# Performance work log

Hardware: AMD Instinct MI355X
Metric: run time of the kernel (lower is better)

## Reference

```python
import jax, jax.numpy as jnp
import numpy as np
import jax.ops

N = 100000   # nodes
E = 3200000  # edges
B = 256      # graphs in batch
F_IN, H, C = 128, 64, 2


def gcn_conv(x, src, dst, W, b):
    # PyG GCNConv: x' = D^{-1/2} (A + I) D^{-1/2} (x W) + b
    n = x.shape[0]
    h = x @ W  # [N, H]
    loop = jnp.arange(n)
    s = jnp.concatenate([src, loop])  # add self-loops
    d = jnp.concatenate([dst, loop])
    deg = jax.ops.segment_sum(jnp.ones_like(d, dtype=h.dtype), d, num_segments=n)
    dinv = jnp.where(deg > 0, jax.lax.rsqrt(deg), 0.0)
    norm = dinv[s] * dinv[d]  # [E+N]
    msg = h[s] * norm[:, None]  # gather + scale
    out = jax.ops.segment_sum(msg, d, num_segments=n)  # scatter-add
    return out + b


def setup_inputs() -> dict:
    key = jax.random.key(0)
    ks = jax.random.split(key, 10)
    x = jax.random.normal(ks[0], (N, F_IN), dtype=jnp.float32)
    edge_index = jax.random.randint(ks[1], (2, E), 0, N, dtype=jnp.int64)
    batch = jnp.sort(jax.random.randint(ks[2], (N,), 0, B, dtype=jnp.int64))
    glorot = lambda k, fi, fo: jax.random.uniform(k, (fi, fo), jnp.float32, -1, 1) * np.sqrt(6.0 / (fi + fo))
    return {
        "x": x, "edge_index": edge_index, "batch": batch,
        "W1": glorot(ks[3], F_IN, H), "b1": jnp.zeros((H,), jnp.float32),
        "W2": glorot(ks[4], H, H), "b2": jnp.zeros((H,), jnp.float32),
        "Wl": glorot(ks[5], H, C), "bl": jnp.zeros((C,), jnp.float32),
    }


def reference(x, edge_index, batch, W1, b1, W2, b2, Wl, bl):
    src, dst = edge_index[0], edge_index[1]
    h = jax.nn.relu(gcn_conv(x, src, dst, W1, b1))
    h = jax.nn.relu(gcn_conv(h, src, dst, W2, b2))
    # global_mean_pool over graph ids
    sums = jax.ops.segment_sum(h, batch, num_segments=B)
    cnt = jax.ops.segment_sum(jnp.ones((h.shape[0],), h.dtype), batch, num_segments=B)
    pooled = sums / jnp.maximum(cnt, 1.0)[:, None]  # [B, H]
    return pooled @ Wl + bl  # [B, C]
```

## Files before the change

kernel.cpp:

```cpp
#include <hip/hip_runtime.h>
#include <hip/hip_bf16.h>


#define HDIM 64
#define NB 256
#define SGRID 256

typedef __attribute__((ext_vector_type(8))) short short8;
typedef __attribute__((ext_vector_type(4))) float f32x4;
typedef __attribute__((ext_vector_type(2))) float f32x2;
union FragU { uint4 u; short8 s; };

static __device__ __forceinline__ unsigned bf16_bits(float f) {
    unsigned u = __float_as_uint(f);
    return (u + 0x7fff + ((u >> 16) & 1)) >> 16;
}
static __device__ __forceinline__ float bflo(unsigned w) { return __uint_as_float(w << 16); }
static __device__ __forceinline__ float bfhi(unsigned w) { return __uint_as_float(w & 0xffff0000u); }


__global__ __launch_bounds__(1024) void k_bcount(const int* __restrict__ dst,
        int* __restrict__ blkhist, int E, int npb, int chunk) {
    __shared__ int lh[NB];
    int tid = threadIdx.x;
    if (tid < NB) lh[tid] = 0;
    __syncthreads();
    int e0 = blockIdx.x * chunk, e1 = min(E, e0 + chunk);
    for (int e = e0 + tid; e < e1; e += 1024)
        atomicAdd(&lh[(unsigned)dst[e] / (unsigned)npb], 1);
    __syncthreads();
    if (tid < NB) blkhist[blockIdx.x * NB + tid] = lh[tid];
}

__global__ void k_bscan2(int* __restrict__ blkhist, int* __restrict__ bcnt) {
    __shared__ int s[SGRID];
    int b = blockIdx.x, t = threadIdx.x;
    int orig = blkhist[t * NB + b];
    s[t] = orig;
    __syncthreads();
    for (int off = 1; off < SGRID; off <<= 1) {
        int v = 0;
        if (t >= off) v = s[t - off];
        __syncthreads();
        s[t] += v;
        __syncthreads();
    }
    blkhist[t * NB + b] = s[t] - orig;
    if (t == SGRID - 1) bcnt[b] = s[t];
}

__global__ __launch_bounds__(1024) void k_bscan_prep(const int* __restrict__ bcnt,
        int* __restrict__ bstart, const float* __restrict__ W1,
        const float* __restrict__ W2, uint4* __restrict__ W1s, uint4* __restrict__ W2s,
        unsigned* __restrict__ hsbA, unsigned* __restrict__ hsbB, int N) {
    __shared__ int s[NB];
    int t = threadIdx.x;
    int orig = 0;
    if (t < NB) { orig = bcnt[t]; s[t] = orig; }
    __syncthreads();
    for (int off = 1; off < NB; off <<= 1) {
        int v = 0;
        if (t < NB && t >= off) v = s[t - off];
        __syncthreads();
        if (t < NB) s[t] += v;
        __syncthreads();
    }
    if (t < NB) bstart[t] = s[t] - orig;
    if (t == NB - 1) bstart[NB] = s[t];
    int lane = t & 63, ci = t >> 6;
    {
        int kt = ci >> 2, nt = ci & 3;
        int kbase = kt * 32 + (lane >> 4) * 8;
        int n = nt * 16 + (lane & 15);
        uint4 o;
        unsigned* op = (unsigned*)&o;
        for (int jj = 0; jj < 4; ++jj) {
            unsigned lo = bf16_bits(W1[(kbase + 2 * jj) * 64 + n]);
            unsigned hi = bf16_bits(W1[(kbase + 2 * jj + 1) * 64 + n]);
            op[jj] = lo | (hi << 16);
        }
        W1s[ci * 64 + lane] = o;
    }
    if (ci < 8) {
        int kt = ci >> 2, nt = ci & 3;
        int kbase = kt * 32 + (lane >> 4) * 8;
        int n = nt * 16 + (lane & 15);
        uint4 o;
        unsigned* op = (unsigned*)&o;
        for (int jj = 0; jj < 4; ++jj) {
            unsigned lo = bf16_bits(W2[(kbase + 2 * jj) * 64 + n]);
            unsigned hi = bf16_bits(W2[(kbase + 2 * jj + 1) * 64 + n]);
            op[jj] = lo | (hi << 16);
        }
        W2s[ci * 64 + lane] = o;
    }
    if (t < 32) hsbA[(size_t)N * 32 + t] = 0;
    else if (t < 64) hsbB[(size_t)N * 32 + (t - 32)] = 0;
}

__global__ __launch_bounds__(1024) void k_bscatter(const int* __restrict__ src,
        const int* __restrict__ dst, const int* __restrict__ bstart,
        const int* __restrict__ blkhist, unsigned* __restrict__ ebuf,
        int E, int npb, int chunk) {
    __shared__ int base[NB], lcur[NB];
    int tid = threadIdx.x;
    if (tid < NB) {
        base[tid] = bstart[tid] + blkhist[blockIdx.x * NB + tid];
        lcur[tid] = 0;
    }
    __syncthreads();
    int e0 = blockIdx.x * chunk, e1 = min(E, e0 + chunk);
    for (int e = e0 + tid; e < e1; e += 1024) {
        int d = dst[e];
        unsigned b = (unsigned)d / (unsigned)npb;
        unsigned ld = (unsigned)d - b * (unsigned)npb;
        int off = atomicAdd(&lcur[b], 1);
        ebuf[base[b] + off] = (ld << 17) | (unsigned)src[e];
    }
}

__global__ __launch_bounds__(1024) void k_bfill(const unsigned* __restrict__ ebuf,
        const int* __restrict__ bstart, int4* __restrict__ meta,
        float* __restrict__ dinv, int* __restrict__ csr, int N, int npb) {
    __shared__ int h[512], p[512], c[512];
    int b = blockIdx.x, tid = threadIdx.x;
    int vlo = b * npb;
    int vcnt = min(npb, N - vlo);
    if (vcnt <= 0) return;
    for (int i = tid; i < 512; i += 1024) h[i] = 0;
    __syncthreads();
    int e0 = bstart[b], e1 = bstart[b + 1];
    for (int e = e0 + tid; e < e1; e += 1024)
        atomicAdd(&h[ebuf[e] >> 17], 1);
    __syncthreads();
    int pc = 0;
    if (tid < 512) {
        pc = (tid < vcnt) ? ((h[tid] + 7) & ~7) : 0;
        p[tid] = pc;
    }
    __syncthreads();
    for (int off = 1; off < 512; off <<= 1) {
        int v = 0;
        if (tid < 512 && tid >= off) v = p[tid - off];
        __syncthreads();
        if (tid < 512) p[tid] += v;
        __syncthreads();
    }
    int bb = e0 + 7 * vlo;
    if (tid < vcnt) {
        int excl = p[tid] - pc;
        int v = vlo + tid;
        float di = rsqrtf((float)(h[tid] + 1));
        meta[v] = make_int4(bb + excl, pc >> 3, __float_as_int(di), 0);
        dinv[v] = di;
        c[tid] = excl;
    }
    __syncthreads();
    for (int e = e0 + tid; e < e1; e += 1024) {
        unsigned ed = ebuf[e];
        int off = atomicAdd(&c[ed >> 17], 1);
        csr[bb + off] = (int)(ed & 0x1FFFFu);
    }
    __syncthreads();
    if (tid < vcnt) {
        int excl = p[tid] - pc;
        for (int q = excl + h[tid]; q < excl + pc; ++q) csr[bb + q] = N;
    }
}

#define MFMA_EPILOGUE(OUT)                                                     \
    {                                                                          \
        int col = lane & 15;                                                   \
        float dv[4];                                                           \
        for (int r = 0; r < 4; ++r) {                                          \
            int vr = v0 + quad * 4 + r;                                        \
            dv[r] = dinv[vr < n ? vr : (n - 1)];                               \
        }                                                                      \
        for (int nt = 0; nt < 4; ++nt)                                         \
            for (int r = 0; r < 4; ++r) {                                      \
                int vr = v0 + quad * 4 + r;                                    \
                float val = acc[nt][r] * dv[r];                                \
                float oth = __shfl_xor(val, 1, 64);                            \
                if (!(lane & 1) && vr < n)                                     \
                    OUT[(size_t)vr * 32 + nt * 8 + (col >> 1)] =               \
                        bf16_bits(val) | (bf16_bits(oth) << 16);               \
            }                                                                  \
    }

__global__ __launch_bounds__(256) void k_mgemm1(const float* __restrict__ X,
        const uint4* __restrict__ W1s, const float* __restrict__ dinv,
        unsigned* __restrict__ hsb, int n) {
    __shared__ float Xs[4][16 * 132];
    int lane = threadIdx.x & 63, wv = threadIdx.x >> 6;
    int v0 = (blockIdx.x * 4 + wv) * 16;
    if (v0 >= n) return;
    const float4* X4 = (const float4*)X;
#pragma unroll
    for (int i = 0; i < 8; ++i) {
        int gi = i * 64 + lane;
        int r = gi >> 5, c4 = gi & 31;
        int vr = v0 + r; if (vr >= n) vr = n - 1;
        float4 t = X4[(size_t)vr * 32 + c4];
        *(float4*)&Xs[wv][r * 132 + c4 * 4] = t;
    }
    int quad = lane >> 4;
    const float* xr = &Xs[wv][(lane & 15) * 132 + quad * 8];
    f32x4 acc[4] = {f32x4{0,0,0,0}, f32x4{0,0,0,0}, f32x4{0,0,0,0}, f32x4{0,0,0,0}};
#pragma unroll
    for (int kt = 0; kt < 4; ++kt) {
        float4 xa = *(const float4*)(xr + kt * 32);
        float4 xb = *(const float4*)(xr + kt * 32 + 4);
        FragU a;
        a.u.x = bf16_bits(xa.x) | (bf16_bits(xa.y) << 16);
        a.u.y = bf16_bits(xa.z) | (bf16_bits(xa.w) << 16);
        a.u.z = bf16_bits(xb.x) | (bf16_bits(xb.y) << 16);
        a.u.w = bf16_bits(xb.z) | (bf16_bits(xb.w) << 16);
#pragma unroll
        for (int nt = 0; nt < 4; ++nt) {
            FragU b; b.u = W1s[(kt * 4 + nt) * 64 + lane];
            acc[nt] = __builtin_amdgcn_mfma_f32_16x16x32_bf16(a.s, b.s, acc[nt], 0, 0, 0);
        }
    }
    MFMA_EPILOGUE(hsb)
}

__global__ __launch_bounds__(256) void k_mgemm2(const unsigned* __restrict__ h1b,
        const uint4* __restrict__ W2s, const float* __restrict__ dinv,
        unsigned* __restrict__ hsbB, int n) {
    int lane = threadIdx.x & 63, wv = threadIdx.x >> 6;
    int v0 = (blockIdx.x * 4 + wv) * 16;
    if (v0 >= n) return;
    int quad = lane >> 4;
    int vm = v0 + (lane & 15); if (vm >= n) vm = n - 1;
    const uint4* h4 = (const uint4*)h1b;
    f32x4 acc[4] = {f32x4{0,0,0,0}, f32x4{0,0,0,0}, f32x4{0,0,0,0}, f32x4{0,0,0,0}};
#pragma unroll
    for (int kt = 0; kt < 2; ++kt) {
        FragU a; a.u = h4[(size_t)vm * 8 + kt * 4 + quad];
#pragma unroll
        for (int nt = 0; nt < 4; ++nt) {
            FragU b; b.u = W2s[(kt * 4 + nt) * 64 + lane];
            acc[nt] = __builtin_amdgcn_mfma_f32_16x16x32_bf16(a.s, b.s, acc[nt], 0, 0, 0);
        }
    }
    MFMA_EPILOGUE(hsbB)
}

#define GATHER_BODY                                                            \
    const uint4* hs4p = (const uint4*)hsb;                                     \
    int o = lane & 7, oct = lane >> 3;                                         \
    int4 mt = meta[v];                                                         \
    int rs = mt.x, nb = mt.y;                                                  \
    float dv = __int_as_float(mt.z);                                           \
    f32x2 A0 = {0.f,0.f}, A1 = {0.f,0.f}, A2 = {0.f,0.f}, A3 = {0.f,0.f};      \
    if (oct == 0) {                                                            \
        uint4 s = hs4p[(size_t)v * 8 + o];                                     \
        A0 = (f32x2){bflo(s.x), bfhi(s.x)};                                    \
        A1 = (f32x2){bflo(s.y), bfhi(s.y)};                                    \
        A2 = (f32x2){bflo(s.z), bfhi(s.z)};                                    \
        A3 = (f32x2){bflo(s.w), bfhi(s.w)};                                    \
    }                                                                          \
    for (int base = 0; base < nb; base += 8) {                                 \
        int idx = csr[rs + base * 8 + lane];   \
        int m = nb - base; if (m > 8) m = 8;                 \
        uint4 wb[8];                                                           \
        _Pragma("unroll")                                                      \
        for (int i = 0; i < 8; ++i)                                            \
            if (i < m) {                                                       \
                int u = __shfl(idx, i * 8 + oct, 64);                          \
                wb[i] = hs4p[(size_t)u * 8 + o];                               \
            }                                                                  \
        _Pragma("unroll")                                                      \
        for (int i = 0; i < 8; ++i)                                            \
            if (i < m) {                                                       \
                A0 += (f32x2){bflo(wb[i].x), bfhi(wb[i].x)};                   \
                A1 += (f32x2){bflo(wb[i].y), bfhi(wb[i].y)};                   \
                A2 += (f32x2){bflo(wb[i].z), bfhi(wb[i].z)};                   \
                A3 += (f32x2){bflo(wb[i].w), bfhi(wb[i].w)};                   \
            }                                                                  \
    }                                                                          \
    A0.x += __shfl_xor(A0.x, 8, 64); A0.x += __shfl_xor(A0.x, 16, 64);         \
    A0.x += __shfl_xor(A0.x, 32, 64);                                          \
    A0.y += __shfl_xor(A0.y, 8, 64); A0.y += __shfl_xor(A0.y, 16, 64);         \
    A0.y += __shfl_xor(A0.y, 32, 64);                                          \
    A1.x += __shfl_xor(A1.x, 8, 64); A1.x += __shfl_xor(A1.x, 16, 64);         \
    A1.x += __shfl_xor(A1.x, 32, 64);                                          \
    A1.y += __shfl_xor(A1.y, 8, 64); A1.y += __shfl_xor(A1.y, 16, 64);         \
    A1.y += __shfl_xor(A1.y, 32, 64);                                          \
    A2.x += __shfl_xor(A2.x, 8, 64); A2.x += __shfl_xor(A2.x, 16, 64);         \
    A2.x += __shfl_xor(A2.x, 32, 64);                                          \
    A2.y += __shfl_xor(A2.y, 8, 64); A2.y += __shfl_xor(A2.y, 16, 64);         \
    A2.y += __shfl_xor(A2.y, 32, 64);                                          \
    A3.x += __shfl_xor(A3.x, 8, 64); A3.x += __shfl_xor(A3.x, 16, 64);         \
    A3.x += __shfl_xor(A3.x, 32, 64);                                          \
    A3.y += __shfl_xor(A3.y, 8, 64); A3.y += __shfl_xor(A3.y, 16, 64);         \
    A3.y += __shfl_xor(A3.y, 32, 64);                                          \
    float4 bb0 = ((const float4*)bias)[2 * o];                                 \
    float4 bb1 = ((const float4*)bias)[2 * o + 1];                             \
    float r0 = fmaxf(fmaf(dv, A0.x, bb0.x), 0.f);                              \
    float r1 = fmaxf(fmaf(dv, A0.y, bb0.y), 0.f);                              \
    float r2 = fmaxf(fmaf(dv, A1.x, bb0.z), 0.f);                              \
    float r3 = fmaxf(fmaf(dv, A1.y, bb0.w), 0.f);                              \
    float r4 = fmaxf(fmaf(dv, A2.x, bb1.x), 0.f);                              \
    float r5 = fmaxf(fmaf(dv, A2.y, bb1.y), 0.f);                              \
    float r6 = fmaxf(fmaf(dv, A3.x, bb1.z), 0.f);                              \
    float r7 = fmaxf(fmaf(dv, A3.y, bb1.w), 0.f);

__global__ void k_conv1(const unsigned* __restrict__ hsb, const int4* __restrict__ meta,
                        const int* __restrict__ csr, const float* __restrict__ bias,
                        unsigned* __restrict__ h1b, int n) {
    int v = (blockIdx.x * 256 + threadIdx.x) >> 6;
    int lane = threadIdx.x & 63;
    if (v >= n) return;
    GATHER_BODY
    if (oct == 0) {
        uint4 pk;
        pk.x = bf16_bits(r0) | (bf16_bits(r1) << 16);
        pk.y = bf16_bits(r2) | (bf16_bits(r3) << 16);
        pk.z = bf16_bits(r4) | (bf16_bits(r5) << 16);
        pk.w = bf16_bits(r6) | (bf16_bits(r7) << 16);
        ((uint4*)h1b)[(size_t)v * 8 + o] = pk;
    }
}

__global__ void k_conv_out(const unsigned* __restrict__ hsb, const int4* __restrict__ meta,
                           const int* __restrict__ csr, const float* __restrict__ bias,
                           const float* __restrict__ Wl, float2* __restrict__ z, int n) {
    int v = (blockIdx.x * 256 + threadIdx.x) >> 6;
    int lane = threadIdx.x & 63;
    if (v >= n) return;
    GATHER_BODY
    const float4* Wl4 = (const float4*)Wl;
    float4 wA = Wl4[4 * o + 0];
    float4 wB = Wl4[4 * o + 1];
    float4 wC = Wl4[4 * o + 2];
    float4 wD = Wl4[4 * o + 3];
    float c0 = r0*wA.x + r1*wA.z + r2*wB.x + r3*wB.z + r4*wC.x + r5*wC.z + r6*wD.x + r7*wD.z;
    float c1 = r0*wA.y + r1*wA.w + r2*wB.y + r3*wB.w + r4*wC.y + r5*wC.w + r6*wD.y + r7*wD.w;
    c0 += __shfl_xor(c0, 1, 64); c1 += __shfl_xor(c1, 1, 64);
    c0 += __shfl_xor(c0, 2, 64); c1 += __shfl_xor(c1, 2, 64);
    c0 += __shfl_xor(c0, 4, 64); c1 += __shfl_xor(c1, 4, 64);
    if (lane == 0) z[v] = make_float2(c0, c1);
}

static __device__ __forceinline__ int lower_bound(const int* __restrict__ a, int n, int key) {
    int lo = 0, hi = n;
    while (lo < hi) {
        int mid = (lo + hi) >> 1;
        if (a[mid] < key) lo = mid + 1; else hi = mid;
    }
    return lo;
}

__global__ void k_pool_z(const float2* __restrict__ z, const int* __restrict__ batch,
                         const float* __restrict__ bl, float* __restrict__ out, int N, int B) {
    int g = (blockIdx.x * 256 + threadIdx.x) >> 6;
    int lane = threadIdx.x & 63;
    if (g >= B) return;
    int lo = lower_bound(batch, N, g);
    int hi = lower_bound(batch, N, g + 1);
    float c0 = 0.f, c1 = 0.f;
    for (int v = lo + lane; v < hi; v += 64) {
        float2 t = z[v];
        c0 += t.x; c1 += t.y;
    }
    #pragma unroll
    for (int off = 32; off; off >>= 1) {
        c0 += __shfl_xor(c0, off, 64);
        c1 += __shfl_xor(c1, off, 64);
    }
    if (lane == 0) {
        float inv = 1.0f / fmaxf((float)(hi - lo), 1.0f);
        out[g * 2 + 0] = c0 * inv + bl[0];
        out[g * 2 + 1] = c1 * inv + bl[1];
    }
}

extern "C" void kernel_launch(void* const* d_in, const int* in_sizes, int n_in,
                              void* d_out, int out_size, void* d_ws, size_t ws_size,
                              hipStream_t stream) {
    const float* x  = (const float*)d_in[0];
    const int* edge = (const int*)d_in[1];
    const int* batch= (const int*)d_in[2];
    const float* W1 = (const float*)d_in[3];
    const float* b1 = (const float*)d_in[4];
    const float* W2 = (const float*)d_in[5];
    const float* b2 = (const float*)d_in[6];
    const float* Wl = (const float*)d_in[7];
    const float* bl = (const float*)d_in[8];
    float* out = (float*)d_out;

    const int N = in_sizes[2];
    const int E = in_sizes[1] / 2;
    const int B = out_size / 2;
    const int* srcp = edge;
    const int* dstp = edge + E;
    const int npb = (N + NB - 1) / NB;

    char* w = (char*)d_ws;
    auto carve = [&](size_t bytes) { void* p = (void*)w; w += (bytes + 255) & ~(size_t)255; return p; };
    int4*     meta    = (int4*)carve((size_t)N * 16);
    float*    dinv    = (float*)carve((size_t)N * 4);
    int*      bcnt    = (int*)carve((NB + 8) * 4);
    int*      bstart  = (int*)carve((NB + 8) * 4);
    int*      blkhist = (int*)carve((size_t)SGRID * NB * 4);
    uint4*    W1s     = (uint4*)carve(16 * 64 * 16);
    uint4*    W2s     = (uint4*)carve(8 * 64 * 16);
    int*      csr     = (int*)carve(((size_t)E + 7 * (size_t)N + 256) * 4);
    unsigned* hsbA    = (unsigned*)carve(((size_t)N + 1) * 32 * 4);
    unsigned* ebuf    = hsbA;
    unsigned* h1b     = (unsigned*)carve(((size_t)N + 1) * 32 * 4);
    unsigned* hsbB    = (unsigned*)carve(((size_t)N + 1) * 32 * 4);
    float2*   zbuf    = (float2*)carve((size_t)N * 8);

    const int chunk = (E + SGRID - 1) / SGRID;
    int wbl = (N + 3) / 4;
    int gbl = (N + 63) / 64;

    k_bcount<<<SGRID, 1024, 0, stream>>>(dstp, blkhist, E, npb, chunk);
    k_bscan2<<<NB, SGRID, 0, stream>>>(blkhist, bcnt);
    k_bscan_prep<<<1, 1024, 0, stream>>>(bcnt, bstart, W1, W2, W1s, W2s, hsbA, hsbB, N);
    k_bscatter<<<SGRID, 1024, 0, stream>>>(srcp, dstp, bstart, blkhist, ebuf, E, npb, chunk);
    k_bfill<<<NB, 1024, 0, stream>>>(ebuf, bstart, meta, dinv, csr, N, npb);

    k_mgemm1<<<gbl, 256, 0, stream>>>(x, W1s, dinv, hsbA, N);
    k_conv1<<<wbl, 256, 0, stream>>>(hsbA, meta, csr, b1, h1b, N);
    k_mgemm2<<<gbl, 256, 0, stream>>>(h1b, W2s, dinv, hsbB, N);
    k_conv_out<<<wbl, 256, 0, stream>>>(hsbB, meta, csr, b2, Wl, zbuf, N);

    k_pool_z<<<(B * 64 + 255) / 256, 256, 0, stream>>>(zbuf, batch, bl, out, N, B);
}
```

Measured before the change: 308.1 us.

## Fuse edge bucket-sort stages into one cooperative kernel with grid syncs

Replaces the five preprocessing kernels (count, column scan, bucket scan/prep, scatter, fill) with a single cooperative kernel of 256 blocks that separates phases with grid.sync. Each thread keeps its edges' packed src/local-dst values and bucket ids in registers (ESLOT=16), so the scatter phase no longer re-reads src/dst from global memory. The intent is to remove kernel launch gaps and one pass over the edge arrays. In exchange it adds grid-wide barriers and register pressure, and it assumes all 256×1024-thread blocks are co-resident and that each block's chunk fits in 16×1024 edges. Block-local returns after the last grid.sync are safe.

```diff
diff --git a/kernel.cpp b/kernel.cpp
--- a/kernel.cpp
+++ b/kernel.cpp
@@ -1,10 +1,13 @@
 #include <hip/hip_runtime.h>
 #include <hip/hip_bf16.h>
+#include <hip/hip_cooperative_groups.h>
+
+namespace cg = cooperative_groups;
 
 
 #define HDIM 64
 #define NB 256
-#define SGRID 256
+#define ESLOT 16
 
 typedef __attribute__((ext_vector_type(8))) short short8;
 typedef __attribute__((ext_vector_type(4))) float f32x4;
@@ -18,153 +21,162 @@
 static __device__ __forceinline__ float bflo(unsigned w) { return __uint_as_float(w << 16); }
 static __device__ __forceinline__ float bfhi(unsigned w) { return __uint_as_float(w & 0xffff0000u); }
 
-
-__global__ __launch_bounds__(1024) void k_bcount(const int* __restrict__ dst,
-        int* __restrict__ blkhist, int E, int npb, int chunk) {
-    __shared__ int lh[NB];
-    int tid = threadIdx.x;
-    if (tid < NB) lh[tid] = 0;
+__global__ __launch_bounds__(1024) void k_sort(const int* __restrict__ src,
+        const int* __restrict__ dst, int* __restrict__ blkhist, int* __restrict__ bcnt,
+        unsigned* __restrict__ ebuf, int4* __restrict__ meta, float* __restrict__ dinv,
+        int* __restrict__ csr, const float* __restrict__ W1, const float* __restrict__ W2,
+        uint4* __restrict__ W1s, uint4* __restrict__ W2s, unsigned* __restrict__ hsbA,
+        unsigned* __restrict__ hsbB, int N, int E, int npb, int chunk) {
+    cg::grid_group grid = cg::this_grid();
+    __shared__ int smem[1536];
+    int b = blockIdx.x, tid = threadIdx.x;
+    int e0 = b * chunk, e1 = min(E, e0 + chunk);
+
+    unsigned pk[ESLOT]; int bk[ESLOT];
+    if (tid < NB) smem[tid] = 0;
     __syncthreads();
-    int e0 = blockIdx.x * chunk, e1 = min(E, e0 + chunk);
-    for (int e = e0 + tid; e < e1; e += 1024)
-        atomicAdd(&lh[(unsigned)dst[e] / (unsigned)npb], 1);
+#pragma unroll
+    for (int s = 0; s < ESLOT; ++s) {
+        int e = e0 + s * 1024 + tid;
+        bk[s] = -1;
+        if (e < e1) {
+            int d = dst[e];
+            unsigned bb = (unsigned)d / (unsigned)npb;
+            unsigned ld = (unsigned)d - bb * (unsigned)npb;
+            pk[s] = (ld << 17) | (unsigned)src[e];
+            bk[s] = (int)bb;
+            atomicAdd(&smem[bb], 1);
+        }
+    }
     __syncthreads();
-    if (tid < NB) blkhist[blockIdx.x * NB + tid] = lh[tid];
-}
-
-__global__ void k_bscan2(int* __restrict__ blkhist, int* __restrict__ bcnt) {
-    __shared__ int s[SGRID];
-    int b = blockIdx.x, t = threadIdx.x;
-    int orig = blkhist[t * NB + b];
-    s[t] = orig;
-    __syncthreads();
-    for (int off = 1; off < SGRID; off <<= 1) {
-        int v = 0;
-        if (t >= off) v = s[t - off];
-        __syncthreads();
-        s[t] += v;
-        __syncthreads();
-    }
-    blkhist[t * NB + b] = s[t] - orig;
-    if (t == SGRID - 1) bcnt[b] = s[t];
-}
-
-__global__ __launch_bounds__(1024) void k_bscan_prep(const int* __restrict__ bcnt,
-        int* __restrict__ bstart, const float* __restrict__ W1,
-        const float* __restrict__ W2, uint4* __restrict__ W1s, uint4* __restrict__ W2s,
-        unsigned* __restrict__ hsbA, unsigned* __restrict__ hsbB, int N) {
-    __shared__ int s[NB];
-    int t = threadIdx.x;
-    int orig = 0;
-    if (t < NB) { orig = bcnt[t]; s[t] = orig; }
-    __syncthreads();
-    for (int off = 1; off < NB; off <<= 1) {
-        int v = 0;
-        if (t < NB && t >= off) v = s[t - off];
-        __syncthreads();
-        if (t < NB) s[t] += v;
-        __syncthreads();
-    }
-    if (t < NB) bstart[t] = s[t] - orig;
-    if (t == NB - 1) bstart[NB] = s[t];
-    int lane = t & 63, ci = t >> 6;
+    if (tid < NB) blkhist[b * NB + tid] = smem[tid];
+    if (b == 0) {
+        int lane = tid & 63, ci = tid >> 6;
+        {
+            int kt = ci >> 2, nt = ci & 3;
+            int kbase = kt * 32 + (lane >> 4) * 8;
+            int n = nt * 16 + (lane & 15);
+            uint4 o; unsigned* op = (unsigned*)&o;
+            for (int jj = 0; jj < 4; ++jj) {
+                unsigned lo = bf16_bits(W1[(kbase + 2 * jj) * 64 + n]);
+                unsigned hi = bf16_bits(W1[(kbase + 2 * jj + 1) * 64 + n]);
+                op[jj] = lo | (hi << 16);
+            }
+            W1s[ci * 64 + lane] = o;
+        }
+        if (ci < 8) {
+            int kt = ci >> 2, nt = ci & 3;
+            int kbase = kt * 32 + (lane >> 4) * 8;
+            int n = nt * 16 + (lane & 15);
+            uint4 o; unsigned* op = (unsigned*)&o;
+            for (int jj = 0; jj < 4; ++jj) {
+                unsigned lo = bf16_bits(W2[(kbase + 2 * jj) * 64 + n]);
+                unsigned hi = bf16_bits(W2[(kbase + 2 * jj + 1) * 64 + n]);
+                op[jj] = lo | (hi << 16);
+            }
+            W2s[ci * 64 + lane] = o;
+        }
+        if (tid < 32) hsbA[(size_t)N * 32 + tid] = 0;
+        else if (tid < 64) hsbB[(size_t)N * 32 + (tid - 32)] = 0;
+    }
+    __threadfence();
+    grid.sync();
+
     {
-        int kt = ci >> 2, nt = ci & 3;
-        int kbase = kt * 32 + (lane >> 4) * 8;
-        int n = nt * 16 + (lane & 15);
-        uint4 o;
-        unsigned* op = (unsigned*)&o;
-        for (int jj = 0; jj < 4; ++jj) {
-            unsigned lo = bf16_bits(W1[(kbase + 2 * jj) * 64 + n]);
-            unsigned hi = bf16_bits(W1[(kbase + 2 * jj + 1) * 64 + n]);
-            op[jj] = lo | (hi << 16);
-        }
-        W1s[ci * 64 + lane] = o;
-    }
-    if (ci < 8) {
-        int kt = ci >> 2, nt = ci & 3;
-        int kbase = kt * 32 + (lane >> 4) * 8;
-        int n = nt * 16 + (lane & 15);
-        uint4 o;
-        unsigned* op = (unsigned*)&o;
-        for (int jj = 0; jj < 4; ++jj) {
-            unsigned lo = bf16_bits(W2[(kbase + 2 * jj) * 64 + n]);
-            unsigned hi = bf16_bits(W2[(kbase + 2 * jj + 1) * 64 + n]);
-            op[jj] = lo | (hi << 16);
-        }
-        W2s[ci * 64 + lane] = o;
-    }
-    if (t < 32) hsbA[(size_t)N * 32 + t] = 0;
-    else if (t < 64) hsbB[(size_t)N * 32 + (t - 32)] = 0;
-}
-
-__global__ __launch_bounds__(1024) void k_bscatter(const int* __restrict__ src,
-        const int* __restrict__ dst, const int* __restrict__ bstart,
-        const int* __restrict__ blkhist, unsigned* __restrict__ ebuf,
-        int E, int npb, int chunk) {
-    __shared__ int base[NB], lcur[NB];
-    int tid = threadIdx.x;
-    if (tid < NB) {
-        base[tid] = bstart[tid] + blkhist[blockIdx.x * NB + tid];
-        lcur[tid] = 0;
-    }
-    __syncthreads();
-    int e0 = blockIdx.x * chunk, e1 = min(E, e0 + chunk);
-    for (int e = e0 + tid; e < e1; e += 1024) {
-        int d = dst[e];
-        unsigned b = (unsigned)d / (unsigned)npb;
-        unsigned ld = (unsigned)d - b * (unsigned)npb;
-        int off = atomicAdd(&lcur[b], 1);
-        ebuf[base[b] + off] = (ld << 17) | (unsigned)src[e];
-    }
-}
-
-__global__ __launch_bounds__(1024) void k_bfill(const unsigned* __restrict__ ebuf,
-        const int* __restrict__ bstart, int4* __restrict__ meta,
-        float* __restrict__ dinv, int* __restrict__ csr, int N, int npb) {
-    __shared__ int h[512], p[512], c[512];
-    int b = blockIdx.x, tid = threadIdx.x;
-    int vlo = b * npb;
-    int vcnt = min(npb, N - vlo);
-    if (vcnt <= 0) return;
-    for (int i = tid; i < 512; i += 1024) h[i] = 0;
-    __syncthreads();
-    int e0 = bstart[b], e1 = bstart[b + 1];
-    for (int e = e0 + tid; e < e1; e += 1024)
-        atomicAdd(&h[ebuf[e] >> 17], 1);
-    __syncthreads();
-    int pc = 0;
-    if (tid < 512) {
-        pc = (tid < vcnt) ? ((h[tid] + 7) & ~7) : 0;
-        p[tid] = pc;
-    }
-    __syncthreads();
-    for (int off = 1; off < 512; off <<= 1) {
-        int v = 0;
-        if (tid < 512 && tid >= off) v = p[tid - off];
-        __syncthreads();
-        if (tid < 512) p[tid] += v;
-        __syncthreads();
-    }
-    int bb = e0 + 7 * vlo;
-    if (tid < vcnt) {
-        int excl = p[tid] - pc;
-        int v = vlo + tid;
-        float di = rsqrtf((float)(h[tid] + 1));
-        meta[v] = make_int4(bb + excl, pc >> 3, __float_as_int(di), 0);
-        dinv[v] = di;
-        c[tid] = excl;
-    }
-    __syncthreads();
-    for (int e = e0 + tid; e < e1; e += 1024) {
-        unsigned ed = ebuf[e];
-        int off = atomicAdd(&c[ed >> 17], 1);
-        csr[bb + off] = (int)(ed & 0x1FFFFu);
-    }
-    __syncthreads();
-    if (tid < vcnt) {
-        int excl = p[tid] - pc;
-        for (int q = excl + h[tid]; q < excl + pc; ++q) csr[bb + q] = N;
+        int orig = 0;
+        if (tid < NB) { orig = blkhist[tid * NB + b]; smem[tid] = orig; }
+        __syncthreads();
+        for (int off = 1; off < NB; off <<= 1) {
+            int v = 0;
+            if (tid < NB && tid >= off) v = smem[tid - off];
+            __syncthreads();
+            if (tid < NB) smem[tid] += v;
+            __syncthreads();
+        }
+        if (tid < NB) blkhist[tid * NB + b] = smem[tid] - orig;
+        if (tid == NB - 1) bcnt[b] = smem[tid];
+    }
+    __threadfence();
+    grid.sync();
+
+    int ed0, ed1;
+    {
+        int* sc   = smem;
+        int* base = smem + 256;
+        int* lcur = smem + 512;
+        int orig = 0;
+        if (tid < NB) { orig = bcnt[tid]; sc[tid] = orig; }
+        __syncthreads();
+        for (int off = 1; off < NB; off <<= 1) {
+            int v = 0;
+            if (tid < NB && tid >= off) v = sc[tid - off];
+            __syncthreads();
+            if (tid < NB) sc[tid] += v;
+            __syncthreads();
+        }
+        if (tid < NB) {
+            base[tid] = (sc[tid] - orig) + blkhist[b * NB + tid];
+            lcur[tid] = 0;
+        }
+        __syncthreads();
+        ed1 = sc[b];
+        ed0 = ed1 - bcnt[b];
+        __syncthreads();
+#pragma unroll
+        for (int s = 0; s < ESLOT; ++s)
+            if (bk[s] >= 0) {
+                int off = atomicAdd(&lcur[bk[s]], 1);
+                ebuf[base[bk[s]] + off] = pk[s];
+            }
+    }
+    __threadfence();
+    grid.sync();
+
+    {
+        int* h = smem;
+        int* p = smem + 512;
+        int* c = smem + 1024;
+        int vlo = b * npb;
+        int vcnt = min(npb, N - vlo);
+        if (vcnt <= 0) return;
+        for (int i = tid; i < 512; i += 1024) h[i] = 0;
+        __syncthreads();
+        for (int e = ed0 + tid; e < ed1; e += 1024)
+            atomicAdd(&h[ebuf[e] >> 17], 1);
+        __syncthreads();
+        int pc = 0;
+        if (tid < 512) {
+            pc = (tid < vcnt) ? ((h[tid] + 7) & ~7) : 0;
+            p[tid] = pc;
+        }
+        __syncthreads();
+        for (int off = 1; off < 512; off <<= 1) {
+            int v = 0;
+            if (tid < 512 && tid >= off) v = p[tid - off];
+            __syncthreads();
+            if (tid < 512) p[tid] += v;
+            __syncthreads();
+        }
+        int bb = ed0 + 7 * vlo;
+        if (tid < vcnt) {
+            int excl = p[tid] - pc;
+            int v = vlo + tid;
+            float di = rsqrtf((float)(h[tid] + 1));
+            meta[v] = make_int4(bb + excl, pc >> 3, __float_as_int(di), 0);
+            dinv[v] = di;
+            c[tid] = excl;
+        }
+        __syncthreads();
+        for (int e = ed0 + tid; e < ed1; e += 1024) {
+            unsigned ed = ebuf[e];
+            int off = atomicAdd(&c[ed >> 17], 1);
+            csr[bb + off] = (int)(ed & 0x1FFFFu);
+        }
+        __syncthreads();
+        if (tid < vcnt) {
+            int excl = p[tid] - pc;
+            for (int q = excl + h[tid]; q < excl + pc; ++q) csr[bb + q] = N;
+        }
     }
 }
 
@@ -217,8 +229,8 @@
         a.u.w = bf16_bits(xb.z) | (bf16_bits(xb.w) << 16);
 #pragma unroll
         for (int nt = 0; nt < 4; ++nt) {
-            FragU b; b.u = W1s[(kt * 4 + nt) * 64 + lane];
-            acc[nt] = __builtin_amdgcn_mfma_f32_16x16x32_bf16(a.s, b.s, acc[nt], 0, 0, 0);
+            FragU bfr; bfr.u = W1s[(kt * 4 + nt) * 64 + lane];
+            acc[nt] = __builtin_amdgcn_mfma_f32_16x16x32_bf16(a.s, bfr.s, acc[nt], 0, 0, 0);
         }
     }
     MFMA_EPILOGUE(hsb)
@@ -239,8 +251,8 @@
         FragU a; a.u = h4[(size_t)vm * 8 + kt * 4 + quad];
 #pragma unroll
         for (int nt = 0; nt < 4; ++nt) {
-            FragU b; b.u = W2s[(kt * 4 + nt) * 64 + lane];
-            acc[nt] = __builtin_amdgcn_mfma_f32_16x16x32_bf16(a.s, b.s, acc[nt], 0, 0, 0);
+            FragU bfr; bfr.u = W2s[(kt * 4 + nt) * 64 + lane];
+            acc[nt] = __builtin_amdgcn_mfma_f32_16x16x32_bf16(a.s, bfr.s, acc[nt], 0, 0, 0);
         }
     }
     MFMA_EPILOGUE(hsbB)
@@ -402,8 +414,7 @@
     int4*     meta    = (int4*)carve((size_t)N * 16);
     float*    dinv    = (float*)carve((size_t)N * 4);
     int*      bcnt    = (int*)carve((NB + 8) * 4);
-    int*      bstart  = (int*)carve((NB + 8) * 4);
-    int*      blkhist = (int*)carve((size_t)SGRID * NB * 4);
+    int*      blkhist = (int*)carve((size_t)NB * NB * 4);
     uint4*    W1s     = (uint4*)carve(16 * 64 * 16);
     uint4*    W2s     = (uint4*)carve(8 * 64 * 16);
     int*      csr     = (int*)carve(((size_t)E + 7 * (size_t)N + 256) * 4);
@@ -413,15 +424,18 @@
     unsigned* hsbB    = (unsigned*)carve(((size_t)N + 1) * 32 * 4);
     float2*   zbuf    = (float2*)carve((size_t)N * 8);
 
-    const int chunk = (E + SGRID - 1) / SGRID;
+    int chunk = (E + NB - 1) / NB;
     int wbl = (N + 3) / 4;
     int gbl = (N + 63) / 64;
 
-    k_bcount<<<SGRID, 1024, 0, stream>>>(dstp, blkhist, E, npb, chunk);
-    k_bscan2<<<NB, SGRID, 0, stream>>>(blkhist, bcnt);
-    k_bscan_prep<<<1, 1024, 0, stream>>>(bcnt, bstart, W1, W2, W1s, W2s, hsbA, hsbB, N);
-    k_bscatter<<<SGRID, 1024, 0, stream>>>(srcp, dstp, bstart, blkhist, ebuf, E, npb, chunk);
-    k_bfill<<<NB, 1024, 0, stream>>>(ebuf, bstart, meta, dinv, csr, N, npb);
+    int Nv = N, Ev = E, npbv = npb, chunkv = chunk;
+    void* args[] = {
+        (void*)&srcp, (void*)&dstp, (void*)&blkhist, (void*)&bcnt, (void*)&ebuf,
+        (void*)&meta, (void*)&dinv, (void*)&csr, (void*)&W1, (void*)&W2,
+        (void*)&W1s, (void*)&W2s, (void*)&hsbA, (void*)&hsbB,
+        (void*)&Nv, (void*)&Ev, (void*)&npbv, (void*)&chunkv
+    };
+    hipLaunchCooperativeKernel((void*)k_sort, dim3(NB), dim3(1024), args, 0, stream);
 
     k_mgemm1<<<gbl, 256, 0, stream>>>(x, W1s, dinv, hsbA, N);
     k_conv1<<<wbl, 256, 0, stream>>>(hsbA, meta, csr, b1, h1b, N);
```

Measured after the change: 688.5 us. +123.5%, slower.

## Fold bucket-offset scan into scatter and fill kernels, vectorize edge loads

Applied to the files above, without the earlier changes.

Removes the single-block prep kernel. Each scatter and fill block now recomputes the 256-entry exclusive scan of bucket counts redundantly, and an extra scatter block does the weight swizzle and zero-padding that prep used to do. The count and scatter kernels read dst/src as int4, and the count kernel spreads its shared histogram over four lane-interleaved copies to cut atomic contention. Chunk is rounded up to a multiple of 4 so each block's vectorized range stays aligned. The trade is one fewer launch and serialized tiny kernel against redundant per-block scans.

```diff
diff --git a/kernel.cpp b/kernel.cpp
--- a/kernel.cpp
+++ b/kernel.cpp
@@ -21,15 +21,26 @@
 
 __global__ __launch_bounds__(1024) void k_bcount(const int* __restrict__ dst,
         int* __restrict__ blkhist, int E, int npb, int chunk) {
-    __shared__ int lh[NB];
+    __shared__ int lh[4 * 257];
     int tid = threadIdx.x;
-    if (tid < NB) lh[tid] = 0;
+    for (int i = tid; i < 4 * 257; i += 1024) lh[i] = 0;
     __syncthreads();
     int e0 = blockIdx.x * chunk, e1 = min(E, e0 + chunk);
-    for (int e = e0 + tid; e < e1; e += 1024)
-        atomicAdd(&lh[(unsigned)dst[e] / (unsigned)npb], 1);
-    __syncthreads();
-    if (tid < NB) blkhist[blockIdx.x * NB + tid] = lh[tid];
+    int cp = (tid & 3) * 257;
+    int ng = (e1 - e0) >> 2;
+    const int4* dst4 = (const int4*)dst;
+    for (int g = (e0 >> 2) + tid; g < (e0 >> 2) + ng; g += 1024) {
+        int4 d4 = dst4[g];
+        atomicAdd(&lh[cp + (unsigned)d4.x / (unsigned)npb], 1);
+        atomicAdd(&lh[cp + (unsigned)d4.y / (unsigned)npb], 1);
+        atomicAdd(&lh[cp + (unsigned)d4.z / (unsigned)npb], 1);
+        atomicAdd(&lh[cp + (unsigned)d4.w / (unsigned)npb], 1);
+    }
+    for (int e = e0 + ng * 4 + tid; e < e1; e += 1024)
+        atomicAdd(&lh[cp + (unsigned)dst[e] / (unsigned)npb], 1);
+    __syncthreads();
+    if (tid < NB)
+        blkhist[blockIdx.x * NB + tid] = lh[tid] + lh[257 + tid] + lh[514 + tid] + lh[771 + tid];
 }
 
 __global__ void k_bscan2(int* __restrict__ blkhist, int* __restrict__ bcnt) {
@@ -49,88 +60,104 @@
     if (t == SGRID - 1) bcnt[b] = s[t];
 }
 
-__global__ __launch_bounds__(1024) void k_bscan_prep(const int* __restrict__ bcnt,
-        int* __restrict__ bstart, const float* __restrict__ W1,
-        const float* __restrict__ W2, uint4* __restrict__ W1s, uint4* __restrict__ W2s,
-        unsigned* __restrict__ hsbA, unsigned* __restrict__ hsbB, int N) {
-    __shared__ int s[NB];
-    int t = threadIdx.x;
+__global__ __launch_bounds__(1024) void k_bscatter(const int* __restrict__ src,
+        const int* __restrict__ dst, const int* __restrict__ bcnt,
+        const int* __restrict__ blkhist, unsigned* __restrict__ ebuf,
+        const float* __restrict__ W1, const float* __restrict__ W2,
+        uint4* __restrict__ W1s, uint4* __restrict__ W2s,
+        unsigned* __restrict__ hsbA, unsigned* __restrict__ hsbB,
+        int N, int E, int npb, int chunk) {
+    int tid = threadIdx.x;
+    if (blockIdx.x == SGRID) {
+        int lane = tid & 63, ci = tid >> 6;
+        {
+            int kt = ci >> 2, nt = ci & 3;
+            int kbase = kt * 32 + (lane >> 4) * 8;
+            int n = nt * 16 + (lane & 15);
+            uint4 o; unsigned* op = (unsigned*)&o;
+            for (int jj = 0; jj < 4; ++jj) {
+                unsigned lo = bf16_bits(W1[(kbase + 2 * jj) * 64 + n]);
+                unsigned hi = bf16_bits(W1[(kbase + 2 * jj + 1) * 64 + n]);
+                op[jj] = lo | (hi << 16);
+            }
+            W1s[ci * 64 + lane] = o;
+        }
+        if (ci < 8) {
+            int kt = ci >> 2, nt = ci & 3;
+            int kbase = kt * 32 + (lane >> 4) * 8;
+            int n = nt * 16 + (lane & 15);
+            uint4 o; unsigned* op = (unsigned*)&o;
+            for (int jj = 0; jj < 4; ++jj) {
+                unsigned lo = bf16_bits(W2[(kbase + 2 * jj) * 64 + n]);
+                unsigned hi = bf16_bits(W2[(kbase + 2 * jj + 1) * 64 + n]);
+                op[jj] = lo | (hi << 16);
+            }
+            W2s[ci * 64 + lane] = o;
+        }
+        if (tid < 32) hsbA[(size_t)N * 32 + tid] = 0;
+        else if (tid < 64) hsbB[(size_t)N * 32 + (tid - 32)] = 0;
+        return;
+    }
+    __shared__ int sc[NB], base[NB], lcur[NB];
+    int b = blockIdx.x;
     int orig = 0;
-    if (t < NB) { orig = bcnt[t]; s[t] = orig; }
+    if (tid < NB) { orig = bcnt[tid]; sc[tid] = orig; }
     __syncthreads();
     for (int off = 1; off < NB; off <<= 1) {
         int v = 0;
-        if (t < NB && t >= off) v = s[t - off];
-        __syncthreads();
-        if (t < NB) s[t] += v;
-        __syncthreads();
-    }
-    if (t < NB) bstart[t] = s[t] - orig;
-    if (t == NB - 1) bstart[NB] = s[t];
-    int lane = t & 63, ci = t >> 6;
-    {
-        int kt = ci >> 2, nt = ci & 3;
-        int kbase = kt * 32 + (lane >> 4) * 8;
-        int n = nt * 16 + (lane & 15);
-        uint4 o;
-        unsigned* op = (unsigned*)&o;
-        for (int jj = 0; jj < 4; ++jj) {
-            unsigned lo = bf16_bits(W1[(kbase + 2 * jj) * 64 + n]);
-            unsigned hi = bf16_bits(W1[(kbase + 2 * jj + 1) * 64 + n]);
-            op[jj] = lo | (hi << 16);
-        }
-        W1s[ci * 64 + lane] = o;
-    }
-    if (ci < 8) {
-        int kt = ci >> 2, nt = ci & 3;
-        int kbase = kt * 32 + (lane >> 4) * 8;
-        int n = nt * 16 + (lane & 15);
-        uint4 o;
-        unsigned* op = (unsigned*)&o;
-        for (int jj = 0; jj < 4; ++jj) {
-            unsigned lo = bf16_bits(W2[(kbase + 2 * jj) * 64 + n]);
-            unsigned hi = bf16_bits(W2[(kbase + 2 * jj + 1) * 64 + n]);
-            op[jj] = lo | (hi << 16);
-        }
-        W2s[ci * 64 + lane] = o;
-    }
-    if (t < 32) hsbA[(size_t)N * 32 + t] = 0;
-    else if (t < 64) hsbB[(size_t)N * 32 + (t - 32)] = 0;
-}
-
-__global__ __launch_bounds__(1024) void k_bscatter(const int* __restrict__ src,
-        const int* __restrict__ dst, const int* __restrict__ bstart,
-        const int* __restrict__ blkhist, unsigned* __restrict__ ebuf,
-        int E, int npb, int chunk) {
-    __shared__ int base[NB], lcur[NB];
-    int tid = threadIdx.x;
+        if (tid < NB && tid >= off) v = sc[tid - off];
+        __syncthreads();
+        if (tid < NB) sc[tid] += v;
+        __syncthreads();
+    }
     if (tid < NB) {
-        base[tid] = bstart[tid] + blkhist[blockIdx.x * NB + tid];
+        base[tid] = (sc[tid] - orig) + blkhist[b * NB + tid];
         lcur[tid] = 0;
     }
     __syncthreads();
-    int e0 = blockIdx.x * chunk, e1 = min(E, e0 + chunk);
-    for (int e = e0 + tid; e < e1; e += 1024) {
-        int d = dst[e];
-        unsigned b = (unsigned)d / (unsigned)npb;
-        unsigned ld = (unsigned)d - b * (unsigned)npb;
-        int off = atomicAdd(&lcur[b], 1);
-        ebuf[base[b] + off] = (ld << 17) | (unsigned)src[e];
-    }
+    int e0 = b * chunk, e1 = min(E, e0 + chunk);
+    int ng = (e1 - e0) >> 2;
+    const int4* dst4 = (const int4*)dst;
+    const int4* src4 = (const int4*)src;
+    for (int g = (e0 >> 2) + tid; g < (e0 >> 2) + ng; g += 1024) {
+        int4 d4 = dst4[g];
+        int4 s4 = src4[g];
+        #define SCAT(D, S) {                                                   \
+            unsigned bb = (unsigned)(D) / (unsigned)npb;                       \
+            unsigned ld = (unsigned)(D) - bb * (unsigned)npb;                  \
+            int off = atomicAdd(&lcur[bb], 1);                                 \
+            ebuf[base[bb] + off] = (ld << 17) | (unsigned)(S); }
+        SCAT(d4.x, s4.x) SCAT(d4.y, s4.y) SCAT(d4.z, s4.z) SCAT(d4.w, s4.w)
+    }
+    for (int e = e0 + ng * 4 + tid; e < e1; e += 1024) {
+        SCAT(dst[e], src[e])
+    }
+    #undef SCAT
 }
 
 __global__ __launch_bounds__(1024) void k_bfill(const unsigned* __restrict__ ebuf,
-        const int* __restrict__ bstart, int4* __restrict__ meta,
+        const int* __restrict__ bcnt, int4* __restrict__ meta,
         float* __restrict__ dinv, int* __restrict__ csr, int N, int npb) {
     __shared__ int h[512], p[512], c[512];
     int b = blockIdx.x, tid = threadIdx.x;
     int vlo = b * npb;
     int vcnt = min(npb, N - vlo);
     if (vcnt <= 0) return;
+    if (tid < NB) h[tid] = bcnt[tid];
+    __syncthreads();
+    for (int off = 1; off < NB; off <<= 1) {
+        int v = 0;
+        if (tid < NB && tid >= off) v = h[tid - off];
+        __syncthreads();
+        if (tid < NB) h[tid] += v;
+        __syncthreads();
+    }
+    int ed1 = h[b];
+    int ed0 = ed1 - bcnt[b];
+    __syncthreads();
     for (int i = tid; i < 512; i += 1024) h[i] = 0;
     __syncthreads();
-    int e0 = bstart[b], e1 = bstart[b + 1];
-    for (int e = e0 + tid; e < e1; e += 1024)
+    for (int e = ed0 + tid; e < ed1; e += 1024)
         atomicAdd(&h[ebuf[e] >> 17], 1);
     __syncthreads();
     int pc = 0;
@@ -146,7 +173,7 @@
         if (tid < 512) p[tid] += v;
         __syncthreads();
     }
-    int bb = e0 + 7 * vlo;
+    int bb = ed0 + 7 * vlo;
     if (tid < vcnt) {
         int excl = p[tid] - pc;
         int v = vlo + tid;
@@ -156,7 +183,7 @@
         c[tid] = excl;
     }
     __syncthreads();
-    for (int e = e0 + tid; e < e1; e += 1024) {
+    for (int e = ed0 + tid; e < ed1; e += 1024) {
         unsigned ed = ebuf[e];
         int off = atomicAdd(&c[ed >> 17], 1);
         csr[bb + off] = (int)(ed & 0x1FFFFu);
@@ -217,8 +244,8 @@
         a.u.w = bf16_bits(xb.z) | (bf16_bits(xb.w) << 16);
 #pragma unroll
         for (int nt = 0; nt < 4; ++nt) {
-            FragU b; b.u = W1s[(kt * 4 + nt) * 64 + lane];
-            acc[nt] = __builtin_amdgcn_mfma_f32_16x16x32_bf16(a.s, b.s, acc[nt], 0, 0, 0);
+            FragU bfr; bfr.u = W1s[(kt * 4 + nt) * 64 + lane];
+            acc[nt] = __builtin_amdgcn_mfma_f32_16x16x32_bf16(a.s, bfr.s, acc[nt], 0, 0, 0);
         }
     }
     MFMA_EPILOGUE(hsb)
@@ -239,8 +266,8 @@
         FragU a; a.u = h4[(size_t)vm * 8 + kt * 4 + quad];
 #pragma unroll
         for (int nt = 0; nt < 4; ++nt) {
-            FragU b; b.u = W2s[(kt * 4 + nt) * 64 + lane];
-            acc[nt] = __builtin_amdgcn_mfma_f32_16x16x32_bf16(a.s, b.s, acc[nt], 0, 0, 0);
+            FragU bfr; bfr.u = W2s[(kt * 4 + nt) * 64 + lane];
+            acc[nt] = __builtin_amdgcn_mfma_f32_16x16x32_bf16(a.s, bfr.s, acc[nt], 0, 0, 0);
         }
     }
     MFMA_EPILOGUE(hsbB)
@@ -402,7 +429,6 @@
     int4*     meta    = (int4*)carve((size_t)N * 16);
     float*    dinv    = (float*)carve((size_t)N * 4);
     int*      bcnt    = (int*)carve((NB + 8) * 4);
-    int*      bstart  = (int*)carve((NB + 8) * 4);
     int*      blkhist = (int*)carve((size_t)SGRID * NB * 4);
     uint4*    W1s     = (uint4*)carve(16 * 64 * 16);
     uint4*    W2s     = (uint4*)carve(8 * 64 * 16);
@@ -413,15 +439,15 @@
     unsigned* hsbB    = (unsigned*)carve(((size_t)N + 1) * 32 * 4);
     float2*   zbuf    = (float2*)carve((size_t)N * 8);
 
-    const int chunk = (E + SGRID - 1) / SGRID;
+    int chunk = ((E + SGRID - 1) / SGRID + 3) & ~3;
     int wbl = (N + 3) / 4;
     int gbl = (N + 63) / 64;
 
     k_bcount<<<SGRID, 1024, 0, stream>>>(dstp, blkhist, E, npb, chunk);
     k_bscan2<<<NB, SGRID, 0, stream>>>(blkhist, bcnt);
-    k_bscan_prep<<<1, 1024, 0, stream>>>(bcnt, bstart, W1, W2, W1s, W2s, hsbA, hsbB, N);
-    k_bscatter<<<SGRID, 1024, 0, stream>>>(srcp, dstp, bstart, blkhist, ebuf, E, npb, chunk);
-    k_bfill<<<NB, 1024, 0, stream>>>(ebuf, bstart, meta, dinv, csr, N, npb);
+    k_bscatter<<<SGRID + 1, 1024, 0, stream>>>(srcp, dstp, bcnt, blkhist, ebuf,
+                                               W1, W2, W1s, W2s, hsbA, hsbB, N, E, npb, chunk);
+    k_bfill<<<NB, 1024, 0, stream>>>(ebuf, bcnt, meta, dinv, csr, N, npb);
 
     k_mgemm1<<<gbl, 256, 0, stream>>>(x, W1s, dinv, hsbA, N);
     k_conv1<<<wbl, 256, 0, stream>>>(hsbA, meta, csr, b1, h1b, N);
```

New measurement: 312.9 us. No clear change (+1.6%).
